# Optimization experiments

Hardware: AMD Instinct MI355X
Metric: run time of the kernel (lower is better)

The kernel has to match this reference:

```python
import jax, jax.numpy as jnp
import numpy as np

BATCH, IN, OUT, P = 8192, 1024, 1024, 8

def setup_inputs() -> dict:
    key = jax.random.key(0)
    k1, k2, k3 = jax.random.split(key, 3)
    x = jax.random.normal(k1, (BATCH, IN), dtype=jnp.float32)
    # per-(output,input) basis coefficients, init ~ randn*0.1 as in torch module
    coefficients = jax.random.normal(k2, (OUT, IN, P), dtype=jnp.float32) * 0.1
    weights = jax.random.normal(k3, (OUT, IN), dtype=jnp.float32)
    return {"x": x, "coefficients": coefficients, "weights": weights}

def reference(x, coefficients, weights):
    # out[b,o] = sum_i x[b,i] * (sum_p coef[o,i,p]) * weights[o,i]
    # == x @ (coef_sum * weights)^T  -- single fused GEMM
    w_eff = coefficients.sum(axis=-1) * weights  # [O, I]
    return jnp.einsum('bi,oi->bo', x, w_eff)
```

## Files before the change

### kernel.cpp

```cpp
#include <hip/hip_runtime.h>
#include <hip/hip_bf16.h>
#include <stdint.h>

#define BATCH 8192
#define IN    1024
#define OUTD  1024
#define PBASIS 8

typedef __attribute__((ext_vector_type(8))) short bf16x8;
typedef __attribute__((ext_vector_type(4))) float floatx4;

__device__ __forceinline__ unsigned short f2bf(float f) {
    union { float f; unsigned u; } v; v.f = f;
    unsigned u = v.u;
    u += 0x7fffu + ((u >> 16) & 1u);
    return (unsigned short)(u >> 16);
}

__global__ void prep_kernel(const float* __restrict__ x,
                            const float* __restrict__ coef,
                            const float* __restrict__ w,
                            unsigned short* __restrict__ xb,
                            unsigned short* __restrict__ weff) {
    int b = blockIdx.x;
    int tid = threadIdx.x;
    if (b < 4096) {
        int idx = b * 256 + tid;
        const float4* p = (const float4*)(x + (size_t)idx * 8);
        float4 a = p[0], c = p[1];
        uint4 o;
        o.x = (unsigned)f2bf(a.x) | ((unsigned)f2bf(a.y) << 16);
        o.y = (unsigned)f2bf(a.z) | ((unsigned)f2bf(a.w) << 16);
        o.z = (unsigned)f2bf(c.x) | ((unsigned)f2bf(c.y) << 16);
        o.w = (unsigned)f2bf(c.z) | ((unsigned)f2bf(c.w) << 16);
        ((uint4*)xb)[idx] = o;
    } else {
        int idx = (b - 4096) * 256 + tid;
        size_t e0 = (size_t)idx * 2;
        const float4* c4 = (const float4*)(coef + e0 * PBASIS);
        float4 a = c4[0], bb = c4[1], c = c4[2], d = c4[3];
        float s0 = (a.x + a.y + a.z + a.w) + (bb.x + bb.y + bb.z + bb.w);
        float s1 = (c.x + c.y + c.z + c.w) + (d.x + d.y + d.z + d.w);
        float2 ww = ((const float2*)w)[idx];
        unsigned b0 = f2bf(s0 * ww.x);
        unsigned b1 = f2bf(s1 * ww.y);
        ((unsigned*)weff)[idx] = b0 | (b1 << 16);
    }
}

__device__ __forceinline__ void gload_lds16(const void* g, void* l) {
    __builtin_amdgcn_global_load_lds(
        (const __attribute__((address_space(1))) unsigned int*)g,
        (__attribute__((address_space(3))) unsigned int*)l,
        16, 0, 0);
}

__global__ __launch_bounds__(256, 2) void gemm_bt(
        const unsigned short* __restrict__ A,
        const unsigned short* __restrict__ B,
        float* __restrict__ C) {
    constexpr int K = IN, BK = 64;
    constexpr int ES = 132;
    __shared__ __align__(16) char smem[32768];
    unsigned short* As = (unsigned short*)smem;
    unsigned short* Bs = As + 128 * BK;
    float* ebuf = (float*)smem;

    const int tid  = threadIdx.x;
    const int bm   = blockIdx.x, bn = blockIdx.y;
    const int lane = tid & 63;
    const int wave = tid >> 6;
    const int wm   = wave & 1, wn = wave >> 1;
    const int t    = lane & 15;
    const int q    = lane >> 4;
    const int r8   = t & 7;

    int g0 = tid,       r0 = g0 >> 3, cs0 = (g0 & 7) ^ (r0 & 7);
    int g1 = 256 + tid, r1 = g1 >> 3, cs1 = (g1 & 7) ^ (r1 & 7);
    int g2 = 512 + tid, r2 = g2 >> 3, cs2 = (g2 & 7) ^ (r2 & 7);
    int g3 = 768 + tid, r3 = g3 >> 3, cs3 = (g3 & 7) ^ (r3 & 7);

    const unsigned short* gA0 = A + (size_t)(bm * 128 + r0) * K + cs0 * 8;
    const unsigned short* gA1 = A + (size_t)(bm * 128 + r1) * K + cs1 * 8;
    const unsigned short* gA2 = A + (size_t)(bm * 128 + r2) * K + cs2 * 8;
    const unsigned short* gA3 = A + (size_t)(bm * 128 + r3) * K + cs3 * 8;
    const unsigned short* gB0 = B + (size_t)(bn * 128 + r0) * K + cs0 * 8;
    const unsigned short* gB1 = B + (size_t)(bn * 128 + r1) * K + cs1 * 8;
    const unsigned short* gB2 = B + (size_t)(bn * 128 + r2) * K + cs2 * 8;
    const unsigned short* gB3 = B + (size_t)(bn * 128 + r3) * K + cs3 * 8;

    unsigned short* dA0 = As + g0 * 8;  unsigned short* dB0 = Bs + g0 * 8;
    unsigned short* dA1 = As + g1 * 8;  unsigned short* dB1 = Bs + g1 * 8;
    unsigned short* dA2 = As + g2 * 8;  unsigned short* dB2 = Bs + g2 * 8;
    unsigned short* dA3 = As + g3 * 8;  unsigned short* dB3 = Bs + g3 * 8;

    const unsigned short* aB0 = As + (wm * 64 + t) * BK + ((0 + q) ^ r8) * 8;
    const unsigned short* aB1 = As + (wm * 64 + t) * BK + ((4 + q) ^ r8) * 8;
    const unsigned short* bB0 = Bs + (wn * 64 + t) * BK + ((0 + q) ^ r8) * 8;
    const unsigned short* bB1 = Bs + (wn * 64 + t) * BK + ((4 + q) ^ r8) * 8;

    floatx4 acc[4][4];
#pragma unroll
    for (int i = 0; i < 4; ++i)
#pragma unroll
        for (int j = 0; j < 4; ++j)
            acc[i][j] = (floatx4){0.f, 0.f, 0.f, 0.f};

#define COMPUTE()                                                   \
    {                                                               \
        bf16x8 af0, af1, af2, af3, ag0, ag1, ag2, ag3;              \
        bf16x8 bf0, bf1, bf2, bf3, bg0, bg1, bg2, bg3;              \
        af0 = *(const bf16x8*)(aB0 + 0 * 1024);                     \
        af1 = *(const bf16x8*)(aB0 + 1 * 1024);                     \
        af2 = *(const bf16x8*)(aB0 + 2 * 1024);                     \
        af3 = *(const bf16x8*)(aB0 + 3 * 1024);                     \
        ag0 = *(const bf16x8*)(aB1 + 0 * 1024);                     \
        ag1 = *(const bf16x8*)(aB1 + 1 * 1024);                     \
        ag2 = *(const bf16x8*)(aB1 + 2 * 1024);                     \
        ag3 = *(const bf16x8*)(aB1 + 3 * 1024);                     \
        bf0 = *(const bf16x8*)(bB0 + 0 * 1024);                     \
        bf1 = *(const bf16x8*)(bB0 + 1 * 1024);                     \
        bf2 = *(const bf16x8*)(bB0 + 2 * 1024);                     \
        bf3 = *(const bf16x8*)(bB0 + 3 * 1024);                     \
        bg0 = *(const bf16x8*)(bB1 + 0 * 1024);                     \
        bg1 = *(const bf16x8*)(bB1 + 1 * 1024);                     \
        bg2 = *(const bf16x8*)(bB1 + 2 * 1024);                     \
        bg3 = *(const bf16x8*)(bB1 + 3 * 1024);                     \
        bf16x8 afv[4] = {af0, af1, af2, af3};                       \
        bf16x8 agv[4] = {ag0, ag1, ag2, ag3};                       \
        bf16x8 bfv[4] = {bf0, bf1, bf2, bf3};                       \
        bf16x8 bgv[4] = {bg0, bg1, bg2, bg3};                       \
        _Pragma("unroll")                                           \
        for (int i = 0; i < 4; ++i)                                 \
            _Pragma("unroll")                                       \
            for (int j = 0; j < 4; ++j) {                           \
                acc[i][j] = __builtin_amdgcn_mfma_f32_16x16x32_bf16(\
                    afv[i], bfv[j], acc[i][j], 0, 0, 0);            \
                acc[i][j] = __builtin_amdgcn_mfma_f32_16x16x32_bf16(\
                    agv[i], bgv[j], acc[i][j], 0, 0, 0);            \
            }                                                       \
    }

    for (int kt = 0; kt < K / BK; ++kt) {
        const int k0 = kt * BK;
        gload_lds16(gA0 + k0, dA0);
        gload_lds16(gA1 + k0, dA1);
        gload_lds16(gA2 + k0, dA2);
        gload_lds16(gA3 + k0, dA3);
        gload_lds16(gB0 + k0, dB0);
        gload_lds16(gB1 + k0, dB1);
        gload_lds16(gB2 + k0, dB2);
        gload_lds16(gB3 + k0, dB3);
        __syncthreads();
        COMPUTE();
        __syncthreads();
    }
#undef COMPUTE

#pragma unroll
    for (int p = 0; p < 4; ++p) {
        if (p) __syncthreads();
        if (wm == (p >> 1)) {
            int dt = p & 1;
#pragma unroll
            for (int half = 0; half < 2; ++half) {
                int tm = dt * 2 + half;
#pragma unroll
                for (int tn = 0; tn < 4; ++tn) {
                    int col = wn * 64 + tn * 16 + t;
#pragma unroll
                    for (int r = 0; r < 4; ++r) {
                        int brow = half * 16 + q * 4 + r;
                        ebuf[brow * ES + col] = acc[tm][tn][r];
                    }
                }
            }
        }
        __syncthreads();
#pragma unroll
        for (int rr = 0; rr < 4; ++rr) {
            int brow = rr * 8 + (tid >> 5);
            int col4 = tid & 31;
            float4 v = *(const float4*)(ebuf + brow * ES + col4 * 4);
            size_t grow = (size_t)(bm * 128 + p * 32 + brow);
            *(float4*)(C + grow * OUTD + bn * 128 + col4 * 4) = v;
        }
    }
}

extern "C" void kernel_launch(void* const* d_in, const int* in_sizes, int n_in,
                              void* d_out, int out_size, void* d_ws, size_t ws_size,
                              hipStream_t stream) {
    const float* x    = (const float*)d_in[0];
    const float* coef = (const float*)d_in[1];
    const float* w    = (const float*)d_in[2];
    float* out = (float*)d_out;

    unsigned short* xb   = (unsigned short*)d_ws;
    unsigned short* weff = (unsigned short*)((char*)d_ws + (size_t)BATCH * IN * 2);

    prep_kernel<<<6144, 256, 0, stream>>>(x, coef, w, xb, weff);
    gemm_bt<<<dim3(BATCH / 128, OUTD / 128), 256, 0, stream>>>(xb, weff, out);
}
```

Baseline: 126.6 us.

## Triple-buffer GEMM LDS stages with async prefetch and a 256x128 tile

```diff
diff --git a/kernel.cpp b/kernel.cpp
--- a/kernel.cpp
+++ b/kernel.cpp
@@ -55,49 +55,51 @@
         16, 0, 0);
 }
 
-__global__ __launch_bounds__(256, 2) void gemm_bt(
+#define BARRIER()  asm volatile("s_barrier" ::: "memory")
+#define WAIT_V6L0() asm volatile("s_waitcnt vmcnt(6) lgkmcnt(0)" ::: "memory")
+#define WAIT_V0L0() asm volatile("s_waitcnt vmcnt(0) lgkmcnt(0)" ::: "memory")
+
+__global__ __launch_bounds__(512, 2) void gemm_bt(
         const unsigned short* __restrict__ A,
         const unsigned short* __restrict__ B,
         float* __restrict__ C) {
-    constexpr int K = IN, BK = 64;
+    constexpr int K = IN, BK = 64, NT = K / BK;
+    constexpr int STG = 49152;
     constexpr int ES = 132;
-    __shared__ __align__(16) char smem[32768];
-    unsigned short* As = (unsigned short*)smem;
-    unsigned short* Bs = As + 128 * BK;
+    __shared__ __align__(16) char smem[3 * STG];
     float* ebuf = (float*)smem;
 
     const int tid  = threadIdx.x;
     const int bm   = blockIdx.x, bn = blockIdx.y;
     const int lane = tid & 63;
     const int wave = tid >> 6;
-    const int wm   = wave & 1, wn = wave >> 1;
+    const int wm   = wave >> 1;
+    const int wn   = wave & 1;
     const int t    = lane & 15;
     const int q    = lane >> 4;
     const int r8   = t & 7;
 
-    int g0 = tid,       r0 = g0 >> 3, cs0 = (g0 & 7) ^ (r0 & 7);
-    int g1 = 256 + tid, r1 = g1 >> 3, cs1 = (g1 & 7) ^ (r1 & 7);
-    int g2 = 512 + tid, r2 = g2 >> 3, cs2 = (g2 & 7) ^ (r2 & 7);
-    int g3 = 768 + tid, r3 = g3 >> 3, cs3 = (g3 & 7) ^ (r3 & 7);
-
-    const unsigned short* gA0 = A + (size_t)(bm * 128 + r0) * K + cs0 * 8;
-    const unsigned short* gA1 = A + (size_t)(bm * 128 + r1) * K + cs1 * 8;
-    const unsigned short* gA2 = A + (size_t)(bm * 128 + r2) * K + cs2 * 8;
-    const unsigned short* gA3 = A + (size_t)(bm * 128 + r3) * K + cs3 * 8;
-    const unsigned short* gB0 = B + (size_t)(bn * 128 + r0) * K + cs0 * 8;
-    const unsigned short* gB1 = B + (size_t)(bn * 128 + r1) * K + cs1 * 8;
-    const unsigned short* gB2 = B + (size_t)(bn * 128 + r2) * K + cs2 * 8;
-    const unsigned short* gB3 = B + (size_t)(bn * 128 + r3) * K + cs3 * 8;
-
-    unsigned short* dA0 = As + g0 * 8;  unsigned short* dB0 = Bs + g0 * 8;
-    unsigned short* dA1 = As + g1 * 8;  unsigned short* dB1 = Bs + g1 * 8;
-    unsigned short* dA2 = As + g2 * 8;  unsigned short* dB2 = Bs + g2 * 8;
-    unsigned short* dA3 = As + g3 * 8;  unsigned short* dB3 = Bs + g3 * 8;
-
-    const unsigned short* aB0 = As + (wm * 64 + t) * BK + ((0 + q) ^ r8) * 8;
-    const unsigned short* aB1 = As + (wm * 64 + t) * BK + ((4 + q) ^ r8) * 8;
-    const unsigned short* bB0 = Bs + (wn * 64 + t) * BK + ((0 + q) ^ r8) * 8;
-    const unsigned short* bB1 = Bs + (wn * 64 + t) * BK + ((4 + q) ^ r8) * 8;
+    int g0 = tid,        ra0 = g0 >> 3, ca0 = (g0 & 7) ^ (ra0 & 7);
+    int g1 = 512 + tid,  ra1 = g1 >> 3, ca1 = (g1 & 7) ^ (ra1 & 7);
+    int g2 = 1024 + tid, ra2 = g2 >> 3, ca2 = (g2 & 7) ^ (ra2 & 7);
+    int g3 = 1536 + tid, ra3 = g3 >> 3, ca3 = (g3 & 7) ^ (ra3 & 7);
+    int h0 = tid,        rb0 = h0 >> 3, cb0 = (h0 & 7) ^ (rb0 & 7);
+    int h1 = 512 + tid,  rb1 = h1 >> 3, cb1 = (h1 & 7) ^ (rb1 & 7);
+
+    const unsigned short* gA0 = A + (size_t)(bm * 256 + ra0) * K + ca0 * 8;
+    const unsigned short* gA1 = A + (size_t)(bm * 256 + ra1) * K + ca1 * 8;
+    const unsigned short* gA2 = A + (size_t)(bm * 256 + ra2) * K + ca2 * 8;
+    const unsigned short* gA3 = A + (size_t)(bm * 256 + ra3) * K + ca3 * 8;
+    const unsigned short* gB0 = B + (size_t)(bn * 128 + rb0) * K + cb0 * 8;
+    const unsigned short* gB1 = B + (size_t)(bn * 128 + rb1) * K + cb1 * 8;
+
+    const int dA0 = g0 * 16, dA1 = g1 * 16, dA2 = g2 * 16, dA3 = g3 * 16;
+    const int dB0 = 32768 + h0 * 16, dB1 = 32768 + h1 * 16;
+
+    const int aO0 = ((wm * 64 + t) * 64 + ((0 + q) ^ r8) * 8) * 2;
+    const int aO1 = ((wm * 64 + t) * 64 + ((4 + q) ^ r8) * 8) * 2;
+    const int bO0 = 32768 + ((wn * 64 + t) * 64 + ((0 + q) ^ r8) * 8) * 2;
+    const int bO1 = 32768 + ((wn * 64 + t) * 64 + ((4 + q) ^ r8) * 8) * 2;
 
     floatx4 acc[4][4];
 #pragma unroll
@@ -106,85 +108,90 @@
         for (int j = 0; j < 4; ++j)
             acc[i][j] = (floatx4){0.f, 0.f, 0.f, 0.f};
 
-#define COMPUTE()                                                   \
+#define STAGE_A3(sp, ko)                                            \
     {                                                               \
-        bf16x8 af0, af1, af2, af3, ag0, ag1, ag2, ag3;              \
-        bf16x8 bf0, bf1, bf2, bf3, bg0, bg1, bg2, bg3;              \
-        af0 = *(const bf16x8*)(aB0 + 0 * 1024);                     \
-        af1 = *(const bf16x8*)(aB0 + 1 * 1024);                     \
-        af2 = *(const bf16x8*)(aB0 + 2 * 1024);                     \
-        af3 = *(const bf16x8*)(aB0 + 3 * 1024);                     \
-        ag0 = *(const bf16x8*)(aB1 + 0 * 1024);                     \
-        ag1 = *(const bf16x8*)(aB1 + 1 * 1024);                     \
-        ag2 = *(const bf16x8*)(aB1 + 2 * 1024);                     \
-        ag3 = *(const bf16x8*)(aB1 + 3 * 1024);                     \
-        bf0 = *(const bf16x8*)(bB0 + 0 * 1024);                     \
-        bf1 = *(const bf16x8*)(bB0 + 1 * 1024);                     \
-        bf2 = *(const bf16x8*)(bB0 + 2 * 1024);                     \
-        bf3 = *(const bf16x8*)(bB0 + 3 * 1024);                     \
-        bg0 = *(const bf16x8*)(bB1 + 0 * 1024);                     \
-        bg1 = *(const bf16x8*)(bB1 + 1 * 1024);                     \
-        bg2 = *(const bf16x8*)(bB1 + 2 * 1024);                     \
-        bg3 = *(const bf16x8*)(bB1 + 3 * 1024);                     \
+        gload_lds16(gA0 + (ko), (sp) + dA0);                        \
+        gload_lds16(gA1 + (ko), (sp) + dA1);                        \
+        gload_lds16(gA2 + (ko), (sp) + dA2);                        \
+    }
+#define STAGE_B3(sp, ko)                                            \
+    {                                                               \
+        gload_lds16(gA3 + (ko), (sp) + dA3);                        \
+        gload_lds16(gB0 + (ko), (sp) + dB0);                        \
+        gload_lds16(gB1 + (ko), (sp) + dB1);                        \
+    }
+#define PHASE(sb, aO, bO)                                           \
+    {                                                               \
+        const char* ab = (sb) + (aO);                               \
+        const char* bb = (sb) + (bO);                               \
+        bf16x8 af0 = *(const bf16x8*)(ab + 0 * 2048);               \
+        bf16x8 af1 = *(const bf16x8*)(ab + 1 * 2048);               \
+        bf16x8 af2 = *(const bf16x8*)(ab + 2 * 2048);               \
+        bf16x8 af3 = *(const bf16x8*)(ab + 3 * 2048);               \
+        bf16x8 bf0 = *(const bf16x8*)(bb + 0 * 2048);               \
+        bf16x8 bf1 = *(const bf16x8*)(bb + 1 * 2048);               \
+        bf16x8 bf2 = *(const bf16x8*)(bb + 2 * 2048);               \
+        bf16x8 bf3 = *(const bf16x8*)(bb + 3 * 2048);               \
         bf16x8 afv[4] = {af0, af1, af2, af3};                       \
-        bf16x8 agv[4] = {ag0, ag1, ag2, ag3};                       \
         bf16x8 bfv[4] = {bf0, bf1, bf2, bf3};                       \
-        bf16x8 bgv[4] = {bg0, bg1, bg2, bg3};                       \
+        __builtin_amdgcn_s_setprio(1);                              \
         _Pragma("unroll")                                           \
         for (int i = 0; i < 4; ++i)                                 \
             _Pragma("unroll")                                       \
-            for (int j = 0; j < 4; ++j) {                           \
+            for (int j = 0; j < 4; ++j)                             \
                 acc[i][j] = __builtin_amdgcn_mfma_f32_16x16x32_bf16(\
                     afv[i], bfv[j], acc[i][j], 0, 0, 0);            \
-                acc[i][j] = __builtin_amdgcn_mfma_f32_16x16x32_bf16(\
-                    agv[i], bgv[j], acc[i][j], 0, 0, 0);            \
-            }                                                       \
-    }
-
-    for (int kt = 0; kt < K / BK; ++kt) {
-        const int k0 = kt * BK;
-        gload_lds16(gA0 + k0, dA0);
-        gload_lds16(gA1 + k0, dA1);
-        gload_lds16(gA2 + k0, dA2);
-        gload_lds16(gA3 + k0, dA3);
-        gload_lds16(gB0 + k0, dB0);
-        gload_lds16(gB1 + k0, dB1);
-        gload_lds16(gB2 + k0, dB2);
-        gload_lds16(gB3 + k0, dB3);
-        __syncthreads();
-        COMPUTE();
-        __syncthreads();
-    }
-#undef COMPUTE
-
-#pragma unroll
-    for (int p = 0; p < 4; ++p) {
-        if (p) __syncthreads();
-        if (wm == (p >> 1)) {
-            int dt = p & 1;
-#pragma unroll
-            for (int half = 0; half < 2; ++half) {
-                int tm = dt * 2 + half;
-#pragma unroll
-                for (int tn = 0; tn < 4; ++tn) {
-                    int col = wn * 64 + tn * 16 + t;
-#pragma unroll
-                    for (int r = 0; r < 4; ++r) {
-                        int brow = half * 16 + q * 4 + r;
-                        ebuf[brow * ES + col] = acc[tm][tn][r];
-                    }
-                }
-            }
-        }
-        __syncthreads();
-#pragma unroll
-        for (int rr = 0; rr < 4; ++rr) {
-            int brow = rr * 8 + (tid >> 5);
-            int col4 = tid & 31;
-            float4 v = *(const float4*)(ebuf + brow * ES + col4 * 4);
-            size_t grow = (size_t)(bm * 128 + p * 32 + brow);
-            *(float4*)(C + grow * OUTD + bn * 128 + col4 * 4) = v;
-        }
+        __builtin_amdgcn_s_setprio(0);                              \
+    }
+
+    {
+        char* s0 = smem;
+        char* s1 = smem + STG;
+        STAGE_A3(s0, 0); STAGE_B3(s0, 0);
+        STAGE_A3(s1, BK); STAGE_B3(s1, BK);
+        WAIT_V6L0();
+        BARRIER();
+    }
+
+    int cur = 0;
+    for (int kt = 0; kt < NT; ++kt) {
+        char* sb = smem + cur * STG;
+        int nx = cur + 2; if (nx >= 3) nx -= 3;
+        char* sp = smem + nx * STG;
+        const int kpre = (kt + 2) * BK;
+        const bool pre = (kt < NT - 2);
+
+        if (pre) STAGE_A3(sp, kpre);
+        PHASE(sb, aO0, bO0);
+        if (pre) STAGE_B3(sp, kpre);
+        PHASE(sb, aO1, bO1);
+
+        if (pre) { WAIT_V6L0(); }
+        else     { WAIT_V0L0(); }
+        BARRIER();
+        ++cur; if (cur == 3) cur = 0;
+    }
+#undef PHASE
+#undef STAGE_A3
+#undef STAGE_B3
+
+    __syncthreads();
+
+#pragma unroll
+    for (int tm = 0; tm < 4; ++tm)
+#pragma unroll
+        for (int tn = 0; tn < 4; ++tn)
+#pragma unroll
+            for (int r = 0; r < 4; ++r)
+                ebuf[(wm * 64 + tm * 16 + q * 4 + r) * ES
+                     + wn * 64 + tn * 16 + t] = acc[tm][tn][r];
+    __syncthreads();
+#pragma unroll
+    for (int ps = 0; ps < 16; ++ps) {
+        int row  = ps * 16 + (tid >> 5);
+        int col4 = tid & 31;
+        float4 v = *(const float4*)(ebuf + row * ES + col4 * 4);
+        *(float4*)(C + (size_t)(bm * 256 + row) * OUTD + bn * 128 + col4 * 4) = v;
     }
 }
 
@@ -200,5 +207,5 @@
     unsigned short* weff = (unsigned short*)((char*)d_ws + (size_t)BATCH * IN * 2);
 
     prep_kernel<<<6144, 256, 0, stream>>>(x, coef, w, xb, weff);
-    gemm_bt<<<dim3(BATCH / 128, OUTD / 128), 256, 0, stream>>>(xb, weff, out);
-}
+    gemm_bt<<<dim3(BATCH / 256, OUTD / 128), 512, 0, stream>>>(xb, weff, out);
+}
```

Measured after the change: 122.5 us. 1.03x faster.
